# Kernel tuning notes

Measured on AMD Instinct MI355X. Metric: run time of the kernel, lower is better.

Reference implementation:

```python
import jax, jax.numpy as jnp
import numpy as np

B, S, D = 8, 2048, 512
UNITS = 512

def setup_inputs() -> dict:
    key = jax.random.key(0)
    k1, k2, k3, k4 = jax.random.split(key, 4)
    x = jax.random.normal(k1, (B, S, D), dtype=jnp.float32)
    # glorot-like scale for weights
    scale = 1.0 / np.sqrt(D)
    W_q = jax.random.normal(k2, (D, UNITS), dtype=jnp.float32) * scale
    W_k = jax.random.normal(k3, (D, UNITS), dtype=jnp.float32) * scale
    W_v = jax.random.normal(k4, (D, UNITS), dtype=jnp.float32) * scale
    return {"x": x, "W_q": W_q, "W_k": W_k, "W_v": W_v}

def reference(x, W_q, W_k, W_v):
    # Q,K,V: [B,S,U]
    Q = jnp.einsum('bsd,du->bsu', x, W_q)
    Km = jnp.einsum('bsd,du->bsu', x, W_k)
    V = jnp.einsum('bsd,du->bsu', x, W_v)
    units = W_q.shape[-1]
    # scores: [B,S,S] = Q @ K^T / sqrt(units)
    scores = jnp.einsum('bqu,bku->bqk', Q, Km) / jnp.sqrt(jnp.float32(units))
    attn = jax.nn.softmax(scores, axis=-1)
    # output: [B,S,U]
    return jnp.einsum('bqk,bku->bqu', attn, V)
```

## Files before the change

kernel.cpp:

```cpp
#include <hip/hip_runtime.h>
#include <math.h>

#define BN 8
#define SN 2048
#define DN 512
#define UN 512
#define MN (BN*SN)

typedef _Float16 f16;
typedef _Float16 f16x8 __attribute__((ext_vector_type(8)));
typedef _Float16 f16x4 __attribute__((ext_vector_type(4)));
typedef _Float16 f16x2 __attribute__((ext_vector_type(2)));
typedef float    f32x4 __attribute__((ext_vector_type(4)));

#define SCALE 0.044194173824159216f
#define LOG2E 1.4426950408889634f
#define DEFER_THR 8.0f

#define CVT_PK(a, b) __builtin_bit_cast(f16x2, __builtin_amdgcn_cvt_pkrtz((a), (b)))

#define BAR_LGKM() do {                                         \
  asm volatile("s_waitcnt lgkmcnt(0)" ::: "memory");            \
  __builtin_amdgcn_s_barrier();                                 \
  __builtin_amdgcn_sched_barrier(0);                            \
} while (0)

__device__ __forceinline__ void gload_lds16(const f16* g, f16* l) {
  __builtin_amdgcn_global_load_lds(
      (const __attribute__((address_space(1))) unsigned int*)g,
      (__attribute__((address_space(3))) unsigned int*)l, 16, 0, 0);
}

__global__ __launch_bounds__(256) void cvt_x_kernel(const float* __restrict__ x,
                                                    f16* __restrict__ x16) {
  int i = (blockIdx.x * 256 + threadIdx.x) * 4;
  float4 v = *(const float4*)(x + i);
  f16x4 o = { (f16)v.x, (f16)v.y, (f16)v.z, (f16)v.w };
  *(f16x4*)(x16 + i) = o;
}

__global__ __launch_bounds__(256) void cvt_w_kernel(const float* __restrict__ Wq,
                                                    const float* __restrict__ Wk,
                                                    const float* __restrict__ Wv,
                                                    f16* __restrict__ Wt) {
  const float* W = blockIdx.y == 0 ? Wq : (blockIdx.y == 1 ? Wk : Wv);
  const float s = blockIdx.y == 0 ? SCALE : 1.0f;
  f16* o = Wt + (size_t)blockIdx.y * DN * UN;
  int t = blockIdx.x * 256 + threadIdx.x;
  int r  = t >> 7;
  int c4 = (t & 127) * 4;
  float4 v = *(const float4*)(W + (size_t)r * UN + c4);
  o[(size_t)(c4 + 0) * DN + r] = (f16)(v.x * s);
  o[(size_t)(c4 + 1) * DN + r] = (f16)(v.y * s);
  o[(size_t)(c4 + 2) * DN + r] = (f16)(v.z * s);
  o[(size_t)(c4 + 3) * DN + r] = (f16)(v.w * s);
}

__global__ __launch_bounds__(256) void qkv_gemm(const f16* __restrict__ x16,
                                                const f16* __restrict__ Wt,
                                                f16* __restrict__ Qh,
                                                f16* __restrict__ Kh,
                                                f16* __restrict__ Vt) {
  __shared__ __align__(16) f16 As[128 * 32];
  __shared__ __align__(16) f16 Bs[128 * 32];

  const int tid = threadIdx.x;
  const int w = tid >> 6, lane = tid & 63;
  const int l15 = lane & 15, lh = lane >> 4;
  const int m0 = blockIdx.x * 128;
  const int n0 = blockIdx.y * 128;
  const int widx = blockIdx.z;
  const f16* Wbase = Wt + (size_t)widx * DN * UN;

  const int wr = (w >> 1) * 64, wc = (w & 1) * 64;
  f32x4 acc[4][4] = {};

  for (int kk = 0; kk < 16; ++kk) {
    const int k0 = kk * 32;
#pragma unroll
    for (int q = 0; q < 2; ++q) {
      int j = q * 256 + tid;
      int r = j >> 2, cs = j & 3;
      int c = cs ^ ((r >> 1) & 3);
      f16* abase = &As[(q * 256 + w * 64) * 8];
      f16* bbase = &Bs[(q * 256 + w * 64) * 8];
      gload_lds16(x16 + (size_t)(m0 + r) * DN + k0 + c * 8, abase);
      gload_lds16(Wbase + (size_t)(n0 + r) * DN + k0 + c * 8, bbase);
    }
    __syncthreads();

    f16x8 a[4], bfr[4];
#pragma unroll
    for (int m = 0; m < 4; ++m) {
      int row = wr + m * 16 + l15;
      int ch = lh ^ ((row >> 1) & 3);
      a[m] = *(const f16x8*)&As[row * 32 + ch * 8];
    }
#pragma unroll
    for (int n = 0; n < 4; ++n) {
      int row = wc + n * 16 + l15;
      int ch = lh ^ ((row >> 1) & 3);
      bfr[n] = *(const f16x8*)&Bs[row * 32 + ch * 8];
    }
#pragma unroll
    for (int m = 0; m < 4; ++m)
#pragma unroll
      for (int n = 0; n < 4; ++n)
        acc[m][n] = __builtin_amdgcn_mfma_f32_16x16x32_f16(a[m], bfr[n], acc[m][n], 0, 0, 0);
    __syncthreads();
  }

  if (widx == 2) {
#pragma unroll
    for (int m = 0; m < 4; ++m) {
      int g = m0 + wr + m * 16 + lh * 4;
      int bb = g >> 11;
      int ss = g & 2047;
#pragma unroll
      for (int n = 0; n < 4; ++n) {
        int u = n0 + wc + n * 16 + l15;
        f16x4 pv = { (f16)acc[m][n][0], (f16)acc[m][n][1],
                     (f16)acc[m][n][2], (f16)acc[m][n][3] };
        *(f16x4*)(Vt + ((size_t)bb * UN + u) * SN + ss) = pv;
      }
    }
  } else {
    f16* O = (widx == 0) ? Qh : Kh;
#pragma unroll
    for (int m = 0; m < 4; ++m)
#pragma unroll
      for (int n = 0; n < 4; ++n)
#pragma unroll
        for (int j = 0; j < 4; ++j)
          O[(size_t)(m0 + wr + m * 16 + lh * 4 + j) * UN + (n0 + wc + n * 16 + l15)] =
              (f16)acc[m][n][j];
  }
}

__global__ __launch_bounds__(512, 2) void attn_kernel(const f16* __restrict__ Qh,
                                                      const f16* __restrict__ Kh,
                                                      const f16* __restrict__ Vt,
                                                      float* __restrict__ out) {
  __shared__ __align__(16) f16 Ks[64 * 512];
  __shared__ __align__(16) f16 Ps[64 * 72];
  __shared__ float redm[2][4][16];
  __shared__ float redl[2][4][16];

  const int tid = threadIdx.x;
  const int w = tid >> 6, lane = tid & 63;
  const int l15 = lane & 15, lh = lane >> 4;
  const int bid = blockIdx.x;
  const int b = bid & 7;
  const int q0 = (bid >> 3) * 64;
  const int rb = w >> 1;
  const int cs = w & 1;

  const f16* Kbat = Kh + (size_t)b * SN * DN;
  const f16* Vbat = Vt + (size_t)b * UN * SN;

  const f16* Qbase = Qh + (size_t)(b * SN + q0 + rb * 16 + l15) * DN;
  f16x8 qf[16];
#pragma unroll
  for (int kc = 0; kc < 16; ++kc)
    qf[kc] = *(const f16x8*)(Qbase + kc * 32 + lh * 8);

  f32x4 acc[4][4] = {};
  float mj[4] = { -1e30f, -1e30f, -1e30f, -1e30f };
  float mrow = -1e30f, lrow = 0.f;

  const f16* vbase = Vbat + (size_t)(w * 64 + l15) * SN + lh * 8;

#pragma unroll
  for (int q = 0; q < 8; ++q) {
    int r = w * 8 + q;
    gload_lds16(Kbat + (size_t)r * DN + (lane ^ (r & 7)) * 8, &Ks[r * 512]);
  }
  f16x8 vreg[4][2];
#pragma unroll
  for (int ut = 0; ut < 4; ++ut)
#pragma unroll
    for (int ks = 0; ks < 2; ++ks)
      vreg[ut][ks] = *(const f16x8*)(vbase + (size_t)(ut * 16) * SN + ks * 32);
  asm volatile("s_waitcnt vmcnt(8)" ::: "memory");
  __builtin_amdgcn_s_barrier();
  __builtin_amdgcn_sched_barrier(0);

  const int kswz = l15 & 7;

  for (int t = 0; t < 32; ++t) {
    const int kv0 = t * 64;

    f32x4 sc0 = {}, sc1 = {};
    const int r0 = cs * 32 + l15;
    __builtin_amdgcn_s_setprio(1);
#pragma unroll
    for (int kc = 0; kc < 16; ++kc) {
      int ch = ((kc * 4 + lh) ^ kswz) * 8;
      f16x8 k0 = *(const f16x8*)&Ks[r0 * 512 + ch];
      f16x8 k1 = *(const f16x8*)&Ks[(r0 + 16) * 512 + ch];
      sc0 = __builtin_amdgcn_mfma_f32_16x16x32_f16(k0, qf[kc], sc0, 0, 0, 0);
      sc1 = __builtin_amdgcn_mfma_f32_16x16x32_f16(k1, qf[kc], sc1, 0, 0, 0);
    }
    __builtin_amdgcn_s_setprio(0);

    float pm = fmaxf(fmaxf(fmaxf(sc0[0], sc0[1]), fmaxf(sc0[2], sc0[3])),
                     fmaxf(fmaxf(sc1[0], sc1[1]), fmaxf(sc1[2], sc1[3])));
    pm = fmaxf(pm, __shfl_xor(pm, 16, 64));
    pm = fmaxf(pm, __shfl_xor(pm, 32, 64));
    if (lh == 0) redm[cs][rb][l15] = pm;
    BAR_LGKM();

    if (t < 31) {
#pragma unroll
      for (int q = 0; q < 8; ++q) {
        int r = w * 8 + q;
        gload_lds16(Kbat + (size_t)(kv0 + 64 + r) * DN + (lane ^ (r & 7)) * 8,
                    &Ks[r * 512]);
      }
    }

    float mn[4];
    bool need = false;
#pragma unroll
    for (int qt = 0; qt < 4; ++qt) {
      mn[qt] = fmaxf(mj[qt], fmaxf(redm[0][qt][l15], redm[1][qt][l15]));
      need = need || (mn[qt] > mj[qt] + DEFER_THR);
    }
    if (__any(need)) {
#pragma unroll
      for (int qt = 0; qt < 4; ++qt) {
        float rs = exp2f((mj[qt] - mn[qt]) * LOG2E);
        mj[qt] = mn[qt];
#pragma unroll
        for (int ut = 0; ut < 4; ++ut) {
          acc[ut][qt][0] *= rs; acc[ut][qt][1] *= rs;
          acc[ut][qt][2] *= rs; acc[ut][qt][3] *= rs;
        }
      }
      float rsr = exp2f((mrow - mj[rb]) * LOG2E);
      mrow = mj[rb];
      lrow *= rsr;
    }

    float p[8];
#pragma unroll
    for (int j = 0; j < 4; ++j) {
      p[j]     = exp2f((sc0[j] - mrow) * LOG2E);
      p[4 + j] = exp2f((sc1[j] - mrow) * LOG2E);
    }
    float ts = (p[0] + p[1]) + (p[2] + p[3]) + (p[4] + p[5]) + (p[6] + p[7]);
    ts += __shfl_xor(ts, 16, 64);
    ts += __shfl_xor(ts, 32, 64);
    lrow += ts;

    const int pbase = (rb * 16 + l15) * 72 + cs * 32 + lh * 4;
    *(f16x2*)&Ps[pbase +  0] = CVT_PK(p[0], p[1]);
    *(f16x2*)&Ps[pbase +  2] = CVT_PK(p[2], p[3]);
    *(f16x2*)&Ps[pbase + 16] = CVT_PK(p[4], p[5]);
    *(f16x2*)&Ps[pbase + 18] = CVT_PK(p[6], p[7]);
    BAR_LGKM();

    __builtin_amdgcn_s_setprio(1);
#pragma unroll
    for (int ks = 0; ks < 2; ++ks) {
#pragma unroll
      for (int qt = 0; qt < 4; ++qt) {
        f16x8 pf = *(const f16x8*)&Ps[(qt * 16 + l15) * 72 + ks * 32 + lh * 8];
#pragma unroll
        for (int ut = 0; ut < 4; ++ut)
          acc[ut][qt] = __builtin_amdgcn_mfma_f32_16x16x32_f16(vreg[ut][ks], pf,
                                                               acc[ut][qt], 0, 0, 0);
      }
    }
    __builtin_amdgcn_s_setprio(0);

    if (t < 31) {
#pragma unroll
      for (int ut = 0; ut < 4; ++ut)
#pragma unroll
        for (int ks = 0; ks < 2; ++ks)
          vreg[ut][ks] = *(const f16x8*)(vbase + (size_t)(ut * 16) * SN +
                                         kv0 + 64 + ks * 32);
      asm volatile("s_waitcnt vmcnt(8)" ::: "memory");
    } else {
      asm volatile("s_waitcnt vmcnt(0)" ::: "memory");
    }
    __builtin_amdgcn_s_barrier();
    __builtin_amdgcn_sched_barrier(0);
  }

  if (lh == 0) redl[cs][rb][l15] = lrow;
  __syncthreads();
#pragma unroll
  for (int qt = 0; qt < 4; ++qt) {
    float linv = 1.0f / (redl[0][qt][l15] + redl[1][qt][l15]);
    float* orow = out + (size_t)(b * SN + q0 + qt * 16 + l15) * UN + w * 64 + lh * 4;
#pragma unroll
    for (int ut = 0; ut < 4; ++ut) {
      f32x4 o = acc[ut][qt];
      o[0] *= linv; o[1] *= linv; o[2] *= linv; o[3] *= linv;
      *(f32x4*)(orow + ut * 16) = o;
    }
  }
}

extern "C" void kernel_launch(void* const* d_in, const int* in_sizes, int n_in,
                              void* d_out, int out_size, void* d_ws, size_t ws_size,
                              hipStream_t stream) {
  const float* x  = (const float*)d_in[0];
  const float* Wq = (const float*)d_in[1];
  const float* Wk = (const float*)d_in[2];
  const float* Wv = (const float*)d_in[3];
  float* out = (float*)d_out;

  f16* x16 = (f16*)d_ws;
  f16* Wt  = x16 + (size_t)MN * DN;
  f16* Qh  = Wt + (size_t)3 * DN * UN;
  f16* Kh  = Qh + (size_t)MN * UN;
  f16* Vt  = Kh + (size_t)MN * UN;

  cvt_x_kernel<<<dim3(MN * DN / 1024), 256, 0, stream>>>(x, x16);
  cvt_w_kernel<<<dim3(256, 3), 256, 0, stream>>>(Wq, Wk, Wv, Wt);
  qkv_gemm<<<dim3(128, 4, 3), 256, 0, stream>>>(x16, Wt, Qh, Kh, Vt);
  attn_kernel<<<256, 512, 0, stream>>>(Qh, Kh, Vt, out);
}
```

Before: 202.9 us.

## Software-pipeline attention loop with double-buffered K and P tiles

The attention loop is restructured so that each iteration computes the Q·K scores for the current tile while running the P·V MFMAs for the previous tile, using double-buffered K and P arrays in LDS. The next K tile's prefetch is issued at the top of the iteration, and the online-softmax rescale of the accumulators is deferred until just before the next P·V step, so one barrier per iteration is removed. The goal is to hide global-load latency and barrier stalls behind matrix work. In exchange, LDS use grows from about 74 KB to about 147 KB per block. That likely allows only one block per CU instead of the two requested by the launch bounds, and adds register pressure plus an epilogue P·V step.

```diff
diff --git a/kernel.cpp b/kernel.cpp
--- a/kernel.cpp
+++ b/kernel.cpp
@@ -141,8 +141,8 @@
                                                       const f16* __restrict__ Kh,
                                                       const f16* __restrict__ Vt,
                                                       float* __restrict__ out) {
-  __shared__ __align__(16) f16 Ks[64 * 512];
-  __shared__ __align__(16) f16 Ps[64 * 72];
+  __shared__ __align__(16) f16 Ks[2][64 * 512];
+  __shared__ __align__(16) f16 Ps[2][64 * 72];
   __shared__ float redm[2][4][16];
   __shared__ float redl[2][4][16];
 
@@ -166,29 +166,36 @@
 
   f32x4 acc[4][4] = {};
   float mj[4] = { -1e30f, -1e30f, -1e30f, -1e30f };
+  float rsA[4] = { 1.f, 1.f, 1.f, 1.f };
+  bool pend = false;
   float mrow = -1e30f, lrow = 0.f;
 
   const f16* vbase = Vbat + (size_t)(w * 64 + l15) * SN + lh * 8;
+  f16x8 vreg[4][2];
 
 #pragma unroll
   for (int q = 0; q < 8; ++q) {
     int r = w * 8 + q;
-    gload_lds16(Kbat + (size_t)r * DN + (lane ^ (r & 7)) * 8, &Ks[r * 512]);
-  }
-  f16x8 vreg[4][2];
-#pragma unroll
-  for (int ut = 0; ut < 4; ++ut)
-#pragma unroll
-    for (int ks = 0; ks < 2; ++ks)
-      vreg[ut][ks] = *(const f16x8*)(vbase + (size_t)(ut * 16) * SN + ks * 32);
-  asm volatile("s_waitcnt vmcnt(8)" ::: "memory");
+    gload_lds16(Kbat + (size_t)r * DN + (lane ^ (r & 7)) * 8, &Ks[0][r * 512]);
+  }
+  asm volatile("s_waitcnt vmcnt(0)" ::: "memory");
   __builtin_amdgcn_s_barrier();
   __builtin_amdgcn_sched_barrier(0);
 
   const int kswz = l15 & 7;
 
   for (int t = 0; t < 32; ++t) {
+    const int cur = t & 1;
     const int kv0 = t * 64;
+
+    if (t < 31) {
+#pragma unroll
+      for (int q = 0; q < 8; ++q) {
+        int r = w * 8 + q;
+        gload_lds16(Kbat + (size_t)(kv0 + 64 + r) * DN + (lane ^ (r & 7)) * 8,
+                    &Ks[cur ^ 1][r * 512]);
+      }
+    }
 
     f32x4 sc0 = {}, sc1 = {};
     const int r0 = cs * 32 + l15;
@@ -196,8 +203,8 @@
 #pragma unroll
     for (int kc = 0; kc < 16; ++kc) {
       int ch = ((kc * 4 + lh) ^ kswz) * 8;
-      f16x8 k0 = *(const f16x8*)&Ks[r0 * 512 + ch];
-      f16x8 k1 = *(const f16x8*)&Ks[(r0 + 16) * 512 + ch];
+      f16x8 k0 = *(const f16x8*)&Ks[cur][r0 * 512 + ch];
+      f16x8 k1 = *(const f16x8*)&Ks[cur][(r0 + 16) * 512 + ch];
       sc0 = __builtin_amdgcn_mfma_f32_16x16x32_f16(k0, qf[kc], sc0, 0, 0, 0);
       sc1 = __builtin_amdgcn_mfma_f32_16x16x32_f16(k1, qf[kc], sc1, 0, 0, 0);
     }
@@ -210,14 +217,37 @@
     if (lh == 0) redm[cs][rb][l15] = pm;
     BAR_LGKM();
 
-    if (t < 31) {
-#pragma unroll
-      for (int q = 0; q < 8; ++q) {
-        int r = w * 8 + q;
-        gload_lds16(Kbat + (size_t)(kv0 + 64 + r) * DN + (lane ^ (r & 7)) * 8,
-                    &Ks[r * 512]);
-      }
-    }
+    if (t > 0) {
+      if (pend) {
+#pragma unroll
+        for (int qt = 0; qt < 4; ++qt)
+#pragma unroll
+          for (int ut = 0; ut < 4; ++ut) {
+            acc[ut][qt][0] *= rsA[qt]; acc[ut][qt][1] *= rsA[qt];
+            acc[ut][qt][2] *= rsA[qt]; acc[ut][qt][3] *= rsA[qt];
+          }
+        pend = false;
+      }
+      __builtin_amdgcn_s_setprio(1);
+#pragma unroll
+      for (int ks = 0; ks < 2; ++ks) {
+#pragma unroll
+        for (int qt = 0; qt < 4; ++qt) {
+          f16x8 pf = *(const f16x8*)&Ps[cur ^ 1][(qt * 16 + l15) * 72 + ks * 32 + lh * 8];
+#pragma unroll
+          for (int ut = 0; ut < 4; ++ut)
+            acc[ut][qt] = __builtin_amdgcn_mfma_f32_16x16x32_f16(vreg[ut][ks], pf,
+                                                                 acc[ut][qt], 0, 0, 0);
+        }
+      }
+      __builtin_amdgcn_s_setprio(0);
+    }
+
+#pragma unroll
+    for (int ut = 0; ut < 4; ++ut)
+#pragma unroll
+      for (int ks = 0; ks < 2; ++ks)
+        vreg[ut][ks] = *(const f16x8*)(vbase + (size_t)(ut * 16) * SN + kv0 + ks * 32);
 
     float mn[4];
     bool need = false;
@@ -229,14 +259,10 @@
     if (__any(need)) {
 #pragma unroll
       for (int qt = 0; qt < 4; ++qt) {
-        float rs = exp2f((mj[qt] - mn[qt]) * LOG2E);
+        rsA[qt] = exp2f((mj[qt] - mn[qt]) * LOG2E);
         mj[qt] = mn[qt];
-#pragma unroll
-        for (int ut = 0; ut < 4; ++ut) {
-          acc[ut][qt][0] *= rs; acc[ut][qt][1] *= rs;
-          acc[ut][qt][2] *= rs; acc[ut][qt][3] *= rs;
-        }
-      }
+      }
+      pend = true;
       float rsr = exp2f((mrow - mj[rb]) * LOG2E);
       mrow = mj[rb];
       lrow *= rsr;
@@ -254,39 +280,35 @@
     lrow += ts;
 
     const int pbase = (rb * 16 + l15) * 72 + cs * 32 + lh * 4;
-    *(f16x2*)&Ps[pbase +  0] = CVT_PK(p[0], p[1]);
-    *(f16x2*)&Ps[pbase +  2] = CVT_PK(p[2], p[3]);
-    *(f16x2*)&Ps[pbase + 16] = CVT_PK(p[4], p[5]);
-    *(f16x2*)&Ps[pbase + 18] = CVT_PK(p[6], p[7]);
-    BAR_LGKM();
-
-    __builtin_amdgcn_s_setprio(1);
-#pragma unroll
-    for (int ks = 0; ks < 2; ++ks) {
-#pragma unroll
-      for (int qt = 0; qt < 4; ++qt) {
-        f16x8 pf = *(const f16x8*)&Ps[(qt * 16 + l15) * 72 + ks * 32 + lh * 8];
-#pragma unroll
-        for (int ut = 0; ut < 4; ++ut)
-          acc[ut][qt] = __builtin_amdgcn_mfma_f32_16x16x32_f16(vreg[ut][ks], pf,
-                                                               acc[ut][qt], 0, 0, 0);
-      }
-    }
-    __builtin_amdgcn_s_setprio(0);
-
-    if (t < 31) {
-#pragma unroll
-      for (int ut = 0; ut < 4; ++ut)
-#pragma unroll
-        for (int ks = 0; ks < 2; ++ks)
-          vreg[ut][ks] = *(const f16x8*)(vbase + (size_t)(ut * 16) * SN +
-                                         kv0 + 64 + ks * 32);
-      asm volatile("s_waitcnt vmcnt(8)" ::: "memory");
-    } else {
-      asm volatile("s_waitcnt vmcnt(0)" ::: "memory");
-    }
+    *(f16x2*)&Ps[cur][pbase +  0] = CVT_PK(p[0], p[1]);
+    *(f16x2*)&Ps[cur][pbase +  2] = CVT_PK(p[2], p[3]);
+    *(f16x2*)&Ps[cur][pbase + 16] = CVT_PK(p[4], p[5]);
+    *(f16x2*)&Ps[cur][pbase + 18] = CVT_PK(p[6], p[7]);
+
+    asm volatile("s_waitcnt vmcnt(8) lgkmcnt(0)" ::: "memory");
     __builtin_amdgcn_s_barrier();
     __builtin_amdgcn_sched_barrier(0);
+  }
+
+  if (pend) {
+#pragma unroll
+    for (int qt = 0; qt < 4; ++qt)
+#pragma unroll
+      for (int ut = 0; ut < 4; ++ut) {
+        acc[ut][qt][0] *= rsA[qt]; acc[ut][qt][1] *= rsA[qt];
+        acc[ut][qt][2] *= rsA[qt]; acc[ut][qt][3] *= rsA[qt];
+      }
+  }
+#pragma unroll
+  for (int ks = 0; ks < 2; ++ks) {
+#pragma unroll
+    for (int qt = 0; qt < 4; ++qt) {
+      f16x8 pf = *(const f16x8*)&Ps[1][(qt * 16 + l15) * 72 + ks * 32 + lh * 8];
+#pragma unroll
+      for (int ut = 0; ut < 4; ++ut)
+        acc[ut][qt] = __builtin_amdgcn_mfma_f32_16x16x32_f16(vreg[ut][ks], pf,
+                                                             acc[ut][qt], 0, 0, 0);
+    }
   }
 
   if (lh == 0) redl[cs][rb][l15] = lrow;
```

Measured after the change: 193.7 us (median of 3 runs). 4.5% less time.
